# Kernel tuning notes

Measured on AMD Instinct MI355X. Metric: run time of the kernel, lower is better.

Reference implementation:

```python
import jax, jax.numpy as jnp
import numpy as np

B, C = 16384, 2048
DELTA_REL = 0.1


def setup_inputs() -> dict:
    key = jax.random.key(0)
    k1, k2, k3 = jax.random.split(key, 3)
    logits = jax.random.normal(k1, (B, C), dtype=jnp.float32)
    u = jax.random.uniform(k2, (B, C), dtype=jnp.float32)
    lab = (jax.random.uniform(k3, (B, C)) > 0.7).astype(jnp.float32)
    targets = jnp.where(u < 0.4, jnp.float32(jnp.nan), lab)
    return {"logits": logits, "targets": targets, "epoch": 3}


def _large_loss_rejection(logits, targets, epoch):
    unknown = jnp.isnan(targets)
    # unknown_to_negative: NaN -> 0 (negative label)
    t = jnp.where(unknown, 0.0, targets)
    # stable BCE-with-logits: softplus(x) - x*t
    losses = jax.nn.softplus(logits) - logits * t

    # --- no-grad mask construction ---
    ul = jax.lax.stop_gradient(losses) * unknown.astype(losses.dtype)
    percent = jnp.minimum(epoch * DELTA_REL, 1.0).astype(jnp.float32)
    n_unknown = jnp.count_nonzero(ul)
    k = jnp.round(n_unknown.astype(jnp.float32) * percent).astype(jnp.int32)
    k = jnp.maximum(k, 1)
    # k-th largest value of flattened unknown losses = topk(k).values.min()
    sorted_desc = jnp.sort(ul.reshape(-1))[::-1]
    loss_threshold = jax.lax.dynamic_slice(sorted_desc, (k - 1,), (1,))[0]
    lambdas = jnp.where(ul > loss_threshold, 0.0, 1.0)

    return losses * lambdas  # reduction='none'


def reference(logits, targets, epoch):
    return _large_loss_rejection(logits, targets, epoch)
```

## Files before the change

### kernel.cpp

```cpp
#include <hip/hip_runtime.h>
#include <math.h>

typedef float    f32x4 __attribute__((ext_vector_type(4)));
typedef unsigned u32x4 __attribute__((ext_vector_type(4)));

#define HC_OFF     0u
#define H12_OFF    16384u
#define H64_OFF    20480u
#define CTRL_OFF   20544u
#define ZERO_WORDS 20560u
#define CAND_OFF   20560u
#define CAND_CAP   900000u
#define LBUF       2048u

#define FLOOR_BITS 0x36000000u

__device__ __forceinline__ float softplus_exact(float x) {
    float ax = fabsf(x);
    float e = (float)exp(-(double)ax);
    float l = (float)log1p((double)e);
    return fmaxf(x, 0.0f) + l;
}
__device__ __forceinline__ unsigned exact_bits(float x) {
    return __float_as_uint(softplus_exact(x));
}

__device__ __forceinline__ unsigned refine_core(float x, float ax, float e,
                                                float sp) {
    unsigned cb = __float_as_uint(sp);
    float mf = 64.0f + 8.0f * ax;
    if (x < 0.0f) mf += __builtin_amdgcn_rcpf(e);
    bool need = (cb < FLOOR_BITS) || (mf >= 524288.0f);
    if (!need) {
        unsigned m = (unsigned)mf;
        unsigned low = cb & 0xFFFFFu;
        need = (low < m) || (low >= 0x100000u - m);
    }
    if (need) cb = exact_bits(x);
    return cb;
}
__device__ __forceinline__ unsigned refine_A(float x, float* spo) {
    float ax = fabsf(x);
    float e = __expf(-ax);
    float sp = fmaxf(x, 0.0f) + __logf(1.0f + e);
    *spo = sp;
    return refine_core(x, ax, e, sp);
}

__device__ __forceinline__ unsigned kA_elem(float x, float t,
                                            unsigned* __restrict__ sh) {
    float ax = fabsf(x);
    float e = __expf(-ax);
    float sp = fmaxf(x, 0.0f) + __logf(1.0f + e);
    unsigned outb;
    if (isnan(t)) {
        unsigned cb = refine_core(x, ax, e, sp);
        if (cb != 0u) atomicAdd(&sh[cb >> 20], 1u);
        outb = cb;
    } else {
        float loss = sp - x * t;
        outb = __float_as_uint(loss) ^ 0x80000000u;
    }
    return outb;
}

__global__ __launch_bounds__(256) void kA_store_hist(
    const float* __restrict__ lg, const float* __restrict__ tg,
    float* __restrict__ out, unsigned* __restrict__ ws, long long n) {
    __shared__ unsigned sh[4096];
    for (int i = threadIdx.x; i < 4096; i += 256) sh[i] = 0;
    __syncthreads();

    long long n8 = n >> 3;
    long long tid = (long long)blockIdx.x * 256 + threadIdx.x;
    long long stride = (long long)gridDim.x * 256;
    const f32x4* lg4 = (const f32x4*)lg;
    const f32x4* tg4 = (const f32x4*)tg;
    f32x4* out4 = (f32x4*)out;

    long long i = tid;
    f32x4 xa, xb, ta, tb;
    if (i < n8) {
        xa = lg4[2 * i];
        xb = lg4[2 * i + 1];
        ta = __builtin_nontemporal_load(&tg4[2 * i]);
        tb = __builtin_nontemporal_load(&tg4[2 * i + 1]);
    }
    while (i < n8) {
        long long j = i + stride;
        f32x4 nxa, nxb, nta, ntb;
        if (j < n8) {
            nxa = lg4[2 * j];
            nxb = lg4[2 * j + 1];
            nta = __builtin_nontemporal_load(&tg4[2 * j]);
            ntb = __builtin_nontemporal_load(&tg4[2 * j + 1]);
        }
        f32x4 oa, ob_;
        oa.x = __uint_as_float(kA_elem(xa.x, ta.x, sh));
        oa.y = __uint_as_float(kA_elem(xa.y, ta.y, sh));
        oa.z = __uint_as_float(kA_elem(xa.z, ta.z, sh));
        oa.w = __uint_as_float(kA_elem(xa.w, ta.w, sh));
        ob_.x = __uint_as_float(kA_elem(xb.x, tb.x, sh));
        ob_.y = __uint_as_float(kA_elem(xb.y, tb.y, sh));
        ob_.z = __uint_as_float(kA_elem(xb.z, tb.z, sh));
        ob_.w = __uint_as_float(kA_elem(xb.w, tb.w, sh));
        out4[2 * i] = oa;
        out4[2 * i + 1] = ob_;
        xa = nxa; xb = nxb; ta = nta; tb = ntb;
        i = j;
    }
    if (tid == 0) {
        for (long long q = (n8 << 3); q < n; ++q)
            out[q] = __uint_as_float(kA_elem(lg[q], tg[q], sh));
    }
    __syncthreads();
    unsigned* hist12 = ws + H12_OFF;
    for (int q = threadIdx.x; q < 4096; q += 256)
        if (sh[q]) atomicAdd(&hist12[q], sh[q]);
}

__global__ __launch_bounds__(256) void k2_sel12(
    unsigned* __restrict__ ws, const int* __restrict__ epoch_ptr) {
    const unsigned* hist12 = ws + H12_OFF;
    unsigned* ctrl = ws + CTRL_OFF;
    __shared__ unsigned long long chunk[256];
    int t = threadIdx.x;
    unsigned long long s = 0;
    for (int j = 0; j < 16; ++j) s += hist12[t * 16 + j];
    chunk[t] = s;
    __syncthreads();
    if (t == 0) {
        unsigned long long tot = 0;
        for (int c = 0; c < 256; ++c) tot += chunk[c];
        int epoch = epoch_ptr[0];
        float percent = fminf((float)epoch * 0.1f, 1.0f);
        float nf = (float)tot;
        float kr = rintf(nf * percent);
        long long k = (long long)kr;
        if (k < 1) k = 1;

        long long cum = 0;
        int b = -1;
        long long kprime = 0;
        for (int c = 255; c >= 0; --c) {
            if (cum + (long long)chunk[c] >= k) {
                long long cc = cum;
                for (int j = 15; j >= 0; --j) {
                    unsigned v = hist12[c * 16 + j];
                    if (cc + (long long)v >= k) {
                        b = c * 16 + j;
                        kprime = k - cc;
                        break;
                    }
                    cc += v;
                }
                break;
            }
            cum += chunk[c];
        }
        ctrl[0] = (unsigned)b;
        ctrl[1] = (unsigned)kprime;
        if (b < 0) {
            ctrl[2] = 0u;
            ctrl[4] = 0xFFFFFFFFu;
            ctrl[6] = 0u;
        } else {
            unsigned lo12 = (unsigned)b << 20;
            double vlo = (double)__uint_as_float(lo12);
            double vhi = (double)__uint_as_float(lo12 + 0xFFFFFu);
            double mb = 1e9;
            if (vlo > 1e-30) {
                double xlo = vlo + log1p(-exp(-vlo)) - 0.001;
                double xhi = vhi + log1p(-exp(-vhi)) + 0.001;
                double axmax = fmax(fabs(xlo), fabs(xhi));
                mb = 64.0 + 8.0 * ceil(axmax);
                if (xlo < 0.0) mb += exp(fmin(-xlo, 30.0));
                mb *= 2.0;
            }
            ctrl[6] = (mb >= 8192.0) ? 8192u : (unsigned)mb;
        }
    }
}

__global__ __launch_bounds__(256) void kB_hist64(
    const float* __restrict__ lg, const unsigned* __restrict__ ob,
    unsigned* __restrict__ ws, long long n) {
    unsigned b12 = ws[CTRL_OFF + 0];
    if (b12 == 0xFFFFFFFFu) return;
    unsigned lo12 = b12 << 20;
    unsigned hi12 = lo12 + (1u << 20);
    unsigned m = ws[CTRL_OFF + 6];

    __shared__ unsigned sh[64];
    __shared__ float buf[LBUF];
    __shared__ unsigned lcnt, gbase;
    if (threadIdx.x < 64) sh[threadIdx.x] = 0;
    if (threadIdx.x == 0) lcnt = 0;
    __syncthreads();

    float* cand = (float*)(ws + CAND_OFF);
    unsigned* cnt = ws + CTRL_OFF + 3;

    long long n4 = n >> 2;
    long long tid = (long long)blockIdx.x * 256 + threadIdx.x;
    long long stride = (long long)gridDim.x * 256;
    const u32x4* o4 = (const u32x4*)ob;

    long long i = tid;
    u32x4 u4;
    if (i < n4) u4 = o4[i];
    while (i < n4) {
        long long j = i + stride;
        u32x4 nu4;
        if (j < n4) nu4 = o4[j];
        unsigned us[4] = {u4.x, u4.y, u4.z, u4.w};
#pragma unroll
        for (int c = 0; c < 4; ++c) {
            unsigned u = us[c];
            if (u != 0u && u >= lo12 && u < hi12) {
                float x = lg[i * 4 + c];
                unsigned rB = u;
                unsigned d = u & 16383u;
                if (d < m || d >= 16384u - m)
                    rB = exact_bits(x);
                atomicAdd(&sh[(rB >> 14) & 63u], 1u);
                unsigned li = atomicAdd(&lcnt, 1u);
                if (li < LBUF) buf[li] = x;
            }
        }
        u4 = nu4;
        i = j;
    }
    if (tid == 0) {
        for (long long q = (n4 << 2); q < n; ++q) {
            unsigned u = ob[q];
            if (u != 0u && u >= lo12 && u < hi12) {
                float x = lg[q];
                unsigned rB = u;
                unsigned d = u & 16383u;
                if (d < m || d >= 16384u - m) rB = exact_bits(x);
                atomicAdd(&sh[(rB >> 14) & 63u], 1u);
                unsigned idx = atomicAdd(cnt, 1u);
                if (idx < CAND_CAP) cand[idx] = x;
            }
        }
    }
    __syncthreads();
    if (threadIdx.x < 64 && sh[threadIdx.x])
        atomicAdd(&ws[H64_OFF + threadIdx.x], sh[threadIdx.x]);
    if (threadIdx.x == 0) {
        unsigned add = (lcnt > LBUF) ? (CAND_CAP + 1u) : lcnt;
        gbase = atomicAdd(cnt, add);
    }
    __syncthreads();
    unsigned c2 = lcnt < LBUF ? lcnt : LBUF;
    for (unsigned q = threadIdx.x; q < c2; q += 256) {
        unsigned gi = gbase + q;
        if (gi < CAND_CAP) cand[gi] = buf[q];
    }
}

__global__ void k4_sel64(unsigned* __restrict__ ws) {
    unsigned* ctrl = ws + CTRL_OFF;
    if (ctrl[0] == 0xFFFFFFFFu) return;
    if (threadIdx.x == 0) {
        long long kprime = (long long)ctrl[1];
        long long cum = 0;
        int s = 0;
        long long kpp = 1;
        for (int j = 63; j >= 0; --j) {
            unsigned v = ws[H64_OFF + j];
            if (cum + (long long)v >= kprime) {
                s = j;
                kpp = kprime - cum;
                break;
            }
            cum += v;
        }
        ctrl[4] = (ctrl[0] << 20) + ((unsigned)s << 14);
        ctrl[5] = (unsigned)kpp;
    }
}

__global__ __launch_bounds__(256) void kC_histwin(
    const float* __restrict__ lg, const unsigned* __restrict__ ob,
    unsigned* __restrict__ ws, long long n) {
    unsigned wlo = ws[CTRL_OFF + 4];
    if (wlo == 0xFFFFFFFFu) return;
    unsigned whi = wlo + 16384u;
    unsigned m = ws[CTRL_OFF + 6];
    unsigned b12 = ws[CTRL_OFF + 0];
    unsigned lo12 = b12 << 20;
    unsigned hi12 = lo12 + (1u << 20);
    unsigned glo = (wlo - lo12 > m) ? wlo - m : lo12;
    unsigned ghi = (hi12 - whi > m) ? whi + m : hi12;
    unsigned count = ws[CTRL_OFF + 3];

    long long tid = (long long)blockIdx.x * 256 + threadIdx.x;
    long long stride = (long long)gridDim.x * 256;

    if (count <= CAND_CAP) {
        const float* cand = (const float*)(ws + CAND_OFF);
        for (long long i = tid; i < (long long)count; i += stride) {
            float x = cand[i];
            float spd;
            unsigned u = refine_A(x, &spd);
            if (u >= glo && u < ghi) {
                unsigned eb = exact_bits(x);
                unsigned rB = u;
                unsigned d = u & 16383u;
                if (d < m || d >= 16384u - m) rB = eb;
                if (rB >= wlo && rB < whi) {
                    unsigned off = eb - wlo;
                    if (off < 16384u) atomicAdd(&ws[HC_OFF + off], 1u);
                }
            }
        }
    } else {
        long long n4 = n >> 2;
        const u32x4* o4 = (const u32x4*)ob;
        for (long long i = tid; i < n4; i += stride) {
            u32x4 u4 = o4[i];
            unsigned us[4] = {u4.x, u4.y, u4.z, u4.w};
#pragma unroll
            for (int c = 0; c < 4; ++c) {
                unsigned u = us[c];
                if (u != 0u && u >= glo && u < ghi) {
                    float x = lg[i * 4 + c];
                    unsigned eb = exact_bits(x);
                    unsigned rB = u;
                    unsigned d = u & 16383u;
                    if (d < m || d >= 16384u - m) rB = eb;
                    if (rB >= wlo && rB < whi) {
                        unsigned off = eb - wlo;
                        if (off < 16384u) atomicAdd(&ws[HC_OFF + off], 1u);
                    }
                }
            }
        }
        if (tid == 0) {
            for (long long i = (n4 << 2); i < n; ++i) {
                unsigned u = ob[i];
                if (u != 0u && u >= glo && u < ghi) {
                    unsigned eb = exact_bits(lg[i]);
                    unsigned rB = u;
                    unsigned d = u & 16383u;
                    if (d < m || d >= 16384u - m) rB = eb;
                    if (rB >= wlo && rB < whi) {
                        unsigned off = eb - wlo;
                        if (off < 16384u) atomicAdd(&ws[HC_OFF + off], 1u);
                    }
                }
            }
        }
    }
}

__global__ __launch_bounds__(1024) void k6_selwin(unsigned* __restrict__ ws) {
    unsigned* ctrl = ws + CTRL_OFF;
    if (ctrl[4] == 0xFFFFFFFFu) return;
    __shared__ unsigned long long csum[1024];
    int t = threadIdx.x;
    unsigned long long s = 0;
    for (int j = 0; j < 16; ++j) s += ws[HC_OFF + t * 16 + j];
    csum[t] = s;
    __syncthreads();
    if (t == 0) {
        long long kpp = (long long)ctrl[5];
        long long cum = 0;
        int sel = 0;
        long long rem = kpp;
        for (int c = 1023; c >= 0; --c) {
            if (cum + (long long)csum[c] >= kpp) {
                sel = c;
                rem = kpp - cum;
                break;
            }
            cum += csum[c];
        }
        long long cc = 0;
        int bsel = 0;
        for (int j = 15; j >= 0; --j) {
            unsigned v = ws[HC_OFF + sel * 16 + j];
            if (cc + (long long)v >= rem) {
                bsel = j;
                break;
            }
            cc += v;
        }
        ctrl[2] = ctrl[4] + (unsigned)(sel * 16 + bsel);
    }
}

__device__ __forceinline__ unsigned kD_elem(unsigned u, unsigned thr,
                                            unsigned m,
                                            const float* __restrict__ lg,
                                            long long idx) {
    if (u & 0x80000000u) return u ^ 0x80000000u;
    unsigned udiff = (u > thr) ? u - thr : thr - u;
    if (udiff <= m) {
        unsigned eb = exact_bits(lg[idx]);
        return (eb > thr) ? 0u : eb;
    }
    return (u > thr) ? 0u : u;
}

__global__ __launch_bounds__(256) void kD_final(
    const float* __restrict__ lg, unsigned* __restrict__ ob,
    const unsigned* __restrict__ ws, long long n) {
    unsigned thr = ws[CTRL_OFF + 2];
    unsigned m = ws[CTRL_OFF + 6];

    long long n8 = n >> 3;
    long long tid = (long long)blockIdx.x * 256 + threadIdx.x;
    long long stride = (long long)gridDim.x * 256;
    u32x4* o4 = (u32x4*)ob;

    long long i = tid;
    u32x4 ua, ub;
    if (i < n8) {
        ua = o4[2 * i];
        ub = o4[2 * i + 1];
    }
    while (i < n8) {
        long long j = i + stride;
        u32x4 nua, nub;
        if (j < n8) {
            nua = o4[2 * j];
            nub = o4[2 * j + 1];
        }
        u32x4 va, vb;
        long long base = i * 8;
        va.x = kD_elem(ua.x, thr, m, lg, base + 0);
        va.y = kD_elem(ua.y, thr, m, lg, base + 1);
        va.z = kD_elem(ua.z, thr, m, lg, base + 2);
        va.w = kD_elem(ua.w, thr, m, lg, base + 3);
        vb.x = kD_elem(ub.x, thr, m, lg, base + 4);
        vb.y = kD_elem(ub.y, thr, m, lg, base + 5);
        vb.z = kD_elem(ub.z, thr, m, lg, base + 6);
        vb.w = kD_elem(ub.w, thr, m, lg, base + 7);
        __builtin_nontemporal_store(va, &o4[2 * i]);
        __builtin_nontemporal_store(vb, &o4[2 * i + 1]);
        ua = nua; ub = nub;
        i = j;
    }
    if (tid == 0) {
        for (long long q = (n8 << 3); q < n; ++q)
            ob[q] = kD_elem(ob[q], thr, m, lg, q);
    }
}

extern "C" void kernel_launch(void* const* d_in, const int* in_sizes, int n_in,
                              void* d_out, int out_size, void* d_ws, size_t ws_size,
                              hipStream_t stream) {
    const float* lg = (const float*)d_in[0];
    const float* tg = (const float*)d_in[1];
    const int* epoch = (const int*)d_in[2];
    float* out = (float*)d_out;
    unsigned* ob = (unsigned*)d_out;
    unsigned* ws = (unsigned*)d_ws;
    long long n = (long long)in_sizes[0];

    (void)hipMemsetAsync(d_ws, 0, (size_t)ZERO_WORDS * 4, stream);

    const int blocks = 2048, threads = 256;
    kA_store_hist<<<blocks, threads, 0, stream>>>(lg, tg, out, ws, n);
    k2_sel12<<<1, 256, 0, stream>>>(ws, epoch);
    kB_hist64<<<blocks, threads, 0, stream>>>(lg, ob, ws, n);
    k4_sel64<<<1, 64, 0, stream>>>(ws);
    kC_histwin<<<1024, threads, 0, stream>>>(lg, ob, ws, n);
    k6_selwin<<<1, 1024, 0, stream>>>(ws);
    kD_final<<<blocks, threads, 0, stream>>>(lg, ob, ws, n);
}
```

Before: 242.0 us.

## Tag unknown losses in LSB to skip unchanged writes in final pass

Changes the intermediate encoding so unknown-label losses carry a set low bit and known losses a cleared low bit, rather than flipping the sign bit on known losses. The final pass can then return known values unchanged and write back only the 16-byte vectors that actually changed, cutting store traffic. The first pass gains a depth-two prefetch when the work divides evenly across the grid. The cost is a one-ULP perturbation of every stored loss, which risks exactness, and the refinement margins are widened by two to absorb it.

```diff
diff --git a/kernel.cpp b/kernel.cpp
--- a/kernel.cpp
+++ b/kernel.cpp
@@ -14,6 +14,7 @@
 #define LBUF       2048u
 
 #define FLOOR_BITS 0x36000000u
+
 
 __device__ __forceinline__ float softplus_exact(float x) {
     float ax = fabsf(x);
@@ -39,11 +40,10 @@
     if (need) cb = exact_bits(x);
     return cb;
 }
-__device__ __forceinline__ unsigned refine_A(float x, float* spo) {
+__device__ __forceinline__ unsigned refine_A(float x) {
     float ax = fabsf(x);
     float e = __expf(-ax);
     float sp = fmaxf(x, 0.0f) + __logf(1.0f + e);
-    *spo = sp;
     return refine_core(x, ax, e, sp);
 }
 
@@ -54,12 +54,12 @@
     float sp = fmaxf(x, 0.0f) + __logf(1.0f + e);
     unsigned outb;
     if (isnan(t)) {
-        unsigned cb = refine_core(x, ax, e, sp);
-        if (cb != 0u) atomicAdd(&sh[cb >> 20], 1u);
+        unsigned cb = refine_core(x, ax, e, sp) | 1u;
+        if (cb != 1u) atomicAdd(&sh[cb >> 20], 1u);
         outb = cb;
     } else {
         float loss = sp - x * t;
-        outb = __float_as_uint(loss) ^ 0x80000000u;
+        outb = __float_as_uint(loss) & ~1u;
     }
     return outb;
 }
@@ -78,39 +78,63 @@
     const f32x4* tg4 = (const f32x4*)tg;
     f32x4* out4 = (f32x4*)out;
 
-    long long i = tid;
-    f32x4 xa, xb, ta, tb;
-    if (i < n8) {
-        xa = lg4[2 * i];
-        xb = lg4[2 * i + 1];
-        ta = __builtin_nontemporal_load(&tg4[2 * i]);
-        tb = __builtin_nontemporal_load(&tg4[2 * i + 1]);
-    }
-    while (i < n8) {
-        long long j = i + stride;
-        f32x4 nxa, nxb, nta, ntb;
-        if (j < n8) {
-            nxa = lg4[2 * j];
-            nxb = lg4[2 * j + 1];
-            nta = __builtin_nontemporal_load(&tg4[2 * j]);
-            ntb = __builtin_nontemporal_load(&tg4[2 * j + 1]);
-        }
-        f32x4 oa, ob_;
-        oa.x = __uint_as_float(kA_elem(xa.x, ta.x, sh));
-        oa.y = __uint_as_float(kA_elem(xa.y, ta.y, sh));
-        oa.z = __uint_as_float(kA_elem(xa.z, ta.z, sh));
-        oa.w = __uint_as_float(kA_elem(xa.w, ta.w, sh));
-        ob_.x = __uint_as_float(kA_elem(xb.x, tb.x, sh));
-        ob_.y = __uint_as_float(kA_elem(xb.y, tb.y, sh));
-        ob_.z = __uint_as_float(kA_elem(xb.z, tb.z, sh));
-        ob_.w = __uint_as_float(kA_elem(xb.w, tb.w, sh));
-        out4[2 * i] = oa;
-        out4[2 * i + 1] = ob_;
-        xa = nxa; xb = nxb; ta = nta; tb = ntb;
-        i = j;
+    if (n8 % stride == 0) {
+        long long iters = n8 / stride;
+        f32x4 xa0, xb0, ta0, tb0, xa1, xb1, ta1, tb1;
+        {
+            long long i = tid;
+            xa0 = lg4[2 * i]; xb0 = lg4[2 * i + 1];
+            ta0 = __builtin_nontemporal_load(&tg4[2 * i]);
+            tb0 = __builtin_nontemporal_load(&tg4[2 * i + 1]);
+        }
+        if (iters > 1) {
+            long long i = tid + stride;
+            xa1 = lg4[2 * i]; xb1 = lg4[2 * i + 1];
+            ta1 = __builtin_nontemporal_load(&tg4[2 * i]);
+            tb1 = __builtin_nontemporal_load(&tg4[2 * i + 1]);
+        }
+        for (long long it = 0; it < iters; ++it) {
+            f32x4 pa, pb, pta, ptb;
+            if (it + 2 < iters) {
+                long long i = tid + (it + 2) * stride;
+                pa = lg4[2 * i]; pb = lg4[2 * i + 1];
+                pta = __builtin_nontemporal_load(&tg4[2 * i]);
+                ptb = __builtin_nontemporal_load(&tg4[2 * i + 1]);
+            }
+            long long i = tid + it * stride;
+            f32x4 oa, ob_;
+            oa.x = __uint_as_float(kA_elem(xa0.x, ta0.x, sh));
+            oa.y = __uint_as_float(kA_elem(xa0.y, ta0.y, sh));
+            oa.z = __uint_as_float(kA_elem(xa0.z, ta0.z, sh));
+            oa.w = __uint_as_float(kA_elem(xa0.w, ta0.w, sh));
+            ob_.x = __uint_as_float(kA_elem(xb0.x, tb0.x, sh));
+            ob_.y = __uint_as_float(kA_elem(xb0.y, tb0.y, sh));
+            ob_.z = __uint_as_float(kA_elem(xb0.z, tb0.z, sh));
+            ob_.w = __uint_as_float(kA_elem(xb0.w, tb0.w, sh));
+            out4[2 * i] = oa;
+            out4[2 * i + 1] = ob_;
+            xa0 = xa1; xb0 = xb1; ta0 = ta1; tb0 = tb1;
+            xa1 = pa; xb1 = pb; ta1 = pta; tb1 = ptb;
+        }
+    } else {
+        for (long long i = tid; i < n8; i += stride) {
+            f32x4 xa = lg4[2 * i], xb = lg4[2 * i + 1];
+            f32x4 ta = tg4[2 * i], tb = tg4[2 * i + 1];
+            f32x4 oa, ob_;
+            oa.x = __uint_as_float(kA_elem(xa.x, ta.x, sh));
+            oa.y = __uint_as_float(kA_elem(xa.y, ta.y, sh));
+            oa.z = __uint_as_float(kA_elem(xa.z, ta.z, sh));
+            oa.w = __uint_as_float(kA_elem(xa.w, ta.w, sh));
+            ob_.x = __uint_as_float(kA_elem(xb.x, tb.x, sh));
+            ob_.y = __uint_as_float(kA_elem(xb.y, tb.y, sh));
+            ob_.z = __uint_as_float(kA_elem(xb.z, tb.z, sh));
+            ob_.w = __uint_as_float(kA_elem(xb.w, tb.w, sh));
+            out4[2 * i] = oa;
+            out4[2 * i + 1] = ob_;
+        }
     }
     if (tid == 0) {
-        for (long long q = (n8 << 3); q < n; ++q)
+        for (long long q = (n >> 3) << 3; q < n; ++q)
             out[q] = __uint_as_float(kA_elem(lg[q], tg[q], sh));
     }
     __syncthreads();
@@ -189,7 +213,7 @@
     if (b12 == 0xFFFFFFFFu) return;
     unsigned lo12 = b12 << 20;
     unsigned hi12 = lo12 + (1u << 20);
-    unsigned m = ws[CTRL_OFF + 6];
+    unsigned medge = ws[CTRL_OFF + 6] + 2u;
 
     __shared__ unsigned sh[64];
     __shared__ float buf[LBUF];
@@ -217,12 +241,12 @@
 #pragma unroll
         for (int c = 0; c < 4; ++c) {
             unsigned u = us[c];
-            if (u != 0u && u >= lo12 && u < hi12) {
+            if ((u & 1u) && u != 1u && u >= lo12 && u < hi12) {
                 float x = lg[i * 4 + c];
                 unsigned rB = u;
                 unsigned d = u & 16383u;
-                if (d < m || d >= 16384u - m)
-                    rB = exact_bits(x);
+                if (d < medge || d >= 16384u - medge)
+                    rB = exact_bits(x) | 1u;
                 atomicAdd(&sh[(rB >> 14) & 63u], 1u);
                 unsigned li = atomicAdd(&lcnt, 1u);
                 if (li < LBUF) buf[li] = x;
@@ -234,11 +258,11 @@
     if (tid == 0) {
         for (long long q = (n4 << 2); q < n; ++q) {
             unsigned u = ob[q];
-            if (u != 0u && u >= lo12 && u < hi12) {
+            if ((u & 1u) && u != 1u && u >= lo12 && u < hi12) {
                 float x = lg[q];
                 unsigned rB = u;
                 unsigned d = u & 16383u;
-                if (d < m || d >= 16384u - m) rB = exact_bits(x);
+                if (d < medge || d >= 16384u - medge) rB = exact_bits(x) | 1u;
                 atomicAdd(&sh[(rB >> 14) & 63u], 1u);
                 unsigned idx = atomicAdd(cnt, 1u);
                 if (idx < CAND_CAP) cand[idx] = x;
@@ -288,12 +312,12 @@
     unsigned wlo = ws[CTRL_OFF + 4];
     if (wlo == 0xFFFFFFFFu) return;
     unsigned whi = wlo + 16384u;
-    unsigned m = ws[CTRL_OFF + 6];
+    unsigned medge = ws[CTRL_OFF + 6] + 2u;
     unsigned b12 = ws[CTRL_OFF + 0];
     unsigned lo12 = b12 << 20;
     unsigned hi12 = lo12 + (1u << 20);
-    unsigned glo = (wlo - lo12 > m) ? wlo - m : lo12;
-    unsigned ghi = (hi12 - whi > m) ? whi + m : hi12;
+    unsigned glo = (wlo - lo12 > medge) ? wlo - medge : lo12;
+    unsigned ghi = (hi12 - whi > medge) ? whi + medge : hi12;
     unsigned count = ws[CTRL_OFF + 3];
 
     long long tid = (long long)blockIdx.x * 256 + threadIdx.x;
@@ -303,13 +327,12 @@
         const float* cand = (const float*)(ws + CAND_OFF);
         for (long long i = tid; i < (long long)count; i += stride) {
             float x = cand[i];
-            float spd;
-            unsigned u = refine_A(x, &spd);
+            unsigned u = refine_A(x) | 1u;
             if (u >= glo && u < ghi) {
                 unsigned eb = exact_bits(x);
                 unsigned rB = u;
                 unsigned d = u & 16383u;
-                if (d < m || d >= 16384u - m) rB = eb;
+                if (d < medge || d >= 16384u - medge) rB = eb | 1u;
                 if (rB >= wlo && rB < whi) {
                     unsigned off = eb - wlo;
                     if (off < 16384u) atomicAdd(&ws[HC_OFF + off], 1u);
@@ -325,12 +348,12 @@
 #pragma unroll
             for (int c = 0; c < 4; ++c) {
                 unsigned u = us[c];
-                if (u != 0u && u >= glo && u < ghi) {
+                if ((u & 1u) && u != 1u && u >= glo && u < ghi) {
                     float x = lg[i * 4 + c];
                     unsigned eb = exact_bits(x);
                     unsigned rB = u;
                     unsigned d = u & 16383u;
-                    if (d < m || d >= 16384u - m) rB = eb;
+                    if (d < medge || d >= 16384u - medge) rB = eb | 1u;
                     if (rB >= wlo && rB < whi) {
                         unsigned off = eb - wlo;
                         if (off < 16384u) atomicAdd(&ws[HC_OFF + off], 1u);
@@ -339,13 +362,13 @@
             }
         }
         if (tid == 0) {
-            for (long long i = (n4 << 2); i < n; ++i) {
-                unsigned u = ob[i];
-                if (u != 0u && u >= glo && u < ghi) {
-                    unsigned eb = exact_bits(lg[i]);
+            for (long long q = (n4 << 2); q < n; ++q) {
+                unsigned u = ob[q];
+                if ((u & 1u) && u != 1u && u >= glo && u < ghi) {
+                    unsigned eb = exact_bits(lg[q]);
                     unsigned rB = u;
                     unsigned d = u & 16383u;
-                    if (d < m || d >= 16384u - m) rB = eb;
+                    if (d < medge || d >= 16384u - medge) rB = eb | 1u;
                     if (rB >= wlo && rB < whi) {
                         unsigned off = eb - wlo;
                         if (off < 16384u) atomicAdd(&ws[HC_OFF + off], 1u);
@@ -393,60 +416,88 @@
 }
 
 __device__ __forceinline__ unsigned kD_elem(unsigned u, unsigned thr,
-                                            unsigned m,
+                                            unsigned mband,
                                             const float* __restrict__ lg,
-                                            long long idx) {
-    if (u & 0x80000000u) return u ^ 0x80000000u;
+                                            long long idx, bool* changed) {
+    if (!(u & 1u)) return u;
     unsigned udiff = (u > thr) ? u - thr : thr - u;
-    if (udiff <= m) {
+    if (udiff <= mband) {
         unsigned eb = exact_bits(lg[idx]);
-        return (eb > thr) ? 0u : eb;
-    }
-    return (u > thr) ? 0u : u;
+        unsigned r = (eb > thr) ? 0u : eb;
+        *changed |= (r != u);
+        return r;
+    }
+    if (u > thr) { *changed = true; return 0u; }
+    return u;
 }
 
 __global__ __launch_bounds__(256) void kD_final(
     const float* __restrict__ lg, unsigned* __restrict__ ob,
     const unsigned* __restrict__ ws, long long n) {
     unsigned thr = ws[CTRL_OFF + 2];
-    unsigned m = ws[CTRL_OFF + 6];
+    unsigned mband = ws[CTRL_OFF + 6] + 2u;
 
     long long n8 = n >> 3;
     long long tid = (long long)blockIdx.x * 256 + threadIdx.x;
     long long stride = (long long)gridDim.x * 256;
     u32x4* o4 = (u32x4*)ob;
 
-    long long i = tid;
-    u32x4 ua, ub;
-    if (i < n8) {
-        ua = o4[2 * i];
-        ub = o4[2 * i + 1];
-    }
-    while (i < n8) {
-        long long j = i + stride;
-        u32x4 nua, nub;
-        if (j < n8) {
-            nua = o4[2 * j];
-            nub = o4[2 * j + 1];
-        }
-        u32x4 va, vb;
-        long long base = i * 8;
-        va.x = kD_elem(ua.x, thr, m, lg, base + 0);
-        va.y = kD_elem(ua.y, thr, m, lg, base + 1);
-        va.z = kD_elem(ua.z, thr, m, lg, base + 2);
-        va.w = kD_elem(ua.w, thr, m, lg, base + 3);
-        vb.x = kD_elem(ub.x, thr, m, lg, base + 4);
-        vb.y = kD_elem(ub.y, thr, m, lg, base + 5);
-        vb.z = kD_elem(ub.z, thr, m, lg, base + 6);
-        vb.w = kD_elem(ub.w, thr, m, lg, base + 7);
-        __builtin_nontemporal_store(va, &o4[2 * i]);
-        __builtin_nontemporal_store(vb, &o4[2 * i + 1]);
-        ua = nua; ub = nub;
-        i = j;
+    if (n8 % stride == 0) {
+        long long iters = n8 / stride;
+        u32x4 ua, ub;
+        {
+            long long i = tid;
+            ua = __builtin_nontemporal_load(&o4[2 * i]);
+            ub = __builtin_nontemporal_load(&o4[2 * i + 1]);
+        }
+        for (long long it = 0; it < iters; ++it) {
+            u32x4 nua, nub;
+            if (it + 1 < iters) {
+                long long j = tid + (it + 1) * stride;
+                nua = __builtin_nontemporal_load(&o4[2 * j]);
+                nub = __builtin_nontemporal_load(&o4[2 * j + 1]);
+            }
+            long long i = tid + it * stride;
+            long long base = i * 8;
+            u32x4 va, vb;
+            bool chA = false, chB = false;
+            va.x = kD_elem(ua.x, thr, mband, lg, base + 0, &chA);
+            va.y = kD_elem(ua.y, thr, mband, lg, base + 1, &chA);
+            va.z = kD_elem(ua.z, thr, mband, lg, base + 2, &chA);
+            va.w = kD_elem(ua.w, thr, mband, lg, base + 3, &chA);
+            vb.x = kD_elem(ub.x, thr, mband, lg, base + 4, &chB);
+            vb.y = kD_elem(ub.y, thr, mband, lg, base + 5, &chB);
+            vb.z = kD_elem(ub.z, thr, mband, lg, base + 6, &chB);
+            vb.w = kD_elem(ub.w, thr, mband, lg, base + 7, &chB);
+            if (chA) __builtin_nontemporal_store(va, &o4[2 * i]);
+            if (chB) __builtin_nontemporal_store(vb, &o4[2 * i + 1]);
+            ua = nua; ub = nub;
+        }
+    } else {
+        for (long long i = tid; i < n8; i += stride) {
+            u32x4 ua = o4[2 * i];
+            u32x4 ub = o4[2 * i + 1];
+            long long base = i * 8;
+            u32x4 va, vb;
+            bool chA = false, chB = false;
+            va.x = kD_elem(ua.x, thr, mband, lg, base + 0, &chA);
+            va.y = kD_elem(ua.y, thr, mband, lg, base + 1, &chA);
+            va.z = kD_elem(ua.z, thr, mband, lg, base + 2, &chA);
+            va.w = kD_elem(ua.w, thr, mband, lg, base + 3, &chA);
+            vb.x = kD_elem(ub.x, thr, mband, lg, base + 4, &chB);
+            vb.y = kD_elem(ub.y, thr, mband, lg, base + 5, &chB);
+            vb.z = kD_elem(ub.z, thr, mband, lg, base + 6, &chB);
+            vb.w = kD_elem(ub.w, thr, mband, lg, base + 7, &chB);
+            if (chA) o4[2 * i] = va;
+            if (chB) o4[2 * i + 1] = vb;
+        }
     }
     if (tid == 0) {
-        for (long long q = (n8 << 3); q < n; ++q)
-            ob[q] = kD_elem(ob[q], thr, m, lg, q);
+        for (long long q = (n >> 3) << 3; q < n; ++q) {
+            bool ch = false;
+            unsigned r = kD_elem(ob[q], thr, mband, lg, q, &ch);
+            if (ch) ob[q] = r;
+        }
     }
 }
 
```

Result: slower. 271.3 us (+12.1%).
